# Performance work log

Measured on AMD Instinct MI355X. Metric: run time of the kernel, lower is better.

Reference implementation:

```python
import jax, jax.numpy as jnp
import numpy as np

N_NODES = 100000
N_EDGES = 3200000
D_FEAT = 32


def setup_inputs() -> dict:
    key = jax.random.key(0)
    k1, k2, k3 = jax.random.split(key, 3)
    inp = jax.random.normal(k1, (N_NODES, D_FEAT), dtype=jnp.float32)
    eidx = jax.random.randint(k2, (2, N_EDGES), 0, N_NODES, dtype=jnp.int64)
    enorm = jax.random.uniform(k3, (N_EDGES,), dtype=jnp.float32)
    esgn = jnp.ones((N_EDGES,), dtype=jnp.float32)
    return {"input": inp, "eidx": eidx, "enorm": enorm, "esgn": esgn}


def reference(input, eidx, enorm, esgn):
    # Gather source node features, scale by sign * norm, scatter-add to targets.
    sidx, tidx = eidx[0], eidx[1]
    message = input[sidx] * (esgn * enorm)[:, None]  # [n_edges, d]
    res = jax.ops.segment_sum(message, tidx, num_segments=input.shape[0])
    return res.astype(input.dtype)
```

## Files before the change

### kernel.cpp

```cpp
#include <hip/hip_runtime.h>


#define G    256
#define KMAX 1024
#define SPAN_SHIFT 7
#define SPAN 128
#define CAP  6144
#define NB   256

__global__ __launch_bounds__(1024) void hist_kernel(
    const int* __restrict__ tidx, int* __restrict__ cnt,
    int n_edges, int epb, int vec)
{
    __shared__ int lh[KMAX];
    int g = blockIdx.x, t = threadIdx.x;
    lh[t] = 0;
    __syncthreads();
    int beg = g * epb;
    int lim = beg + epb; if (lim > n_edges) lim = n_edges;
    if (vec) {
        int nq = (lim > beg) ? ((lim - beg) >> 2) : 0;
        for (int q = t; q < nq; q += 1024) {
            int4 tn = *(const int4*)(tidx + beg + q * 4);
            atomicAdd(&lh[tn.x >> SPAN_SHIFT], 1);
            atomicAdd(&lh[tn.y >> SPAN_SHIFT], 1);
            atomicAdd(&lh[tn.z >> SPAN_SHIFT], 1);
            atomicAdd(&lh[tn.w >> SPAN_SHIFT], 1);
        }
        for (int e = beg + (nq << 2) + t; e < lim; e += 1024)
            atomicAdd(&lh[tidx[e] >> SPAN_SHIFT], 1);
    } else {
        for (int e = beg + t; e < lim; e += 1024)
            atomicAdd(&lh[tidx[e] >> SPAN_SHIFT], 1);
    }
    __syncthreads();
    cnt[g * KMAX + t] = lh[t];
}

__global__ __launch_bounds__(G) void scan1_kernel(
    const int* __restrict__ cnt, int* __restrict__ pref, int* __restrict__ tot)
{
    __shared__ int part[G];
    int b = blockIdx.x, t = threadIdx.x;
    int c = cnt[t * KMAX + b];
    part[t] = c;
    __syncthreads();
    for (int off = 1; off < G; off <<= 1) {
        int v = (t >= off) ? part[t - off] : 0;
        __syncthreads();
        part[t] += v;
        __syncthreads();
    }
    pref[t * KMAX + b] = part[t] - c;
    if (t == G - 1) tot[b] = part[t];
}

__global__ __launch_bounds__(KMAX) void bscan_kernel(
    const int* __restrict__ tot, int* __restrict__ bbase)
{
    __shared__ int part[KMAX];
    int t = threadIdx.x;
    int c = tot[t];
    part[t] = c;
    __syncthreads();
    for (int off = 1; off < KMAX; off <<= 1) {
        int v = (t >= off) ? part[t - off] : 0;
        __syncthreads();
        part[t] += v;
        __syncthreads();
    }
    bbase[t] = part[t] - c;
    if (t == KMAX - 1) bbase[KMAX] = part[t];
}

__global__ __launch_bounds__(1024) void scatter_kernel(
    const int* __restrict__ sidx, const int* __restrict__ tidx,
    const float* __restrict__ enorm, const float* __restrict__ esgn,
    const int* __restrict__ bbase, const int* __restrict__ pref,
    int2* __restrict__ recs, int n_edges, int epb, int vec)
{
    __shared__ int gbase[KMAX];
    __shared__ int lh[KMAX];
    int g = blockIdx.x, t = threadIdx.x;
    gbase[t] = bbase[t] + pref[g * KMAX + t];
    lh[t] = 0;
    __syncthreads();
    int beg = g * epb;
    int lim = beg + epb; if (lim > n_edges) lim = n_edges;

    #define SCAT_EDGE(tn_, sn_, w_) {                                        \
        int b_ = (tn_) >> SPAN_SHIFT;                                        \
        int rank_ = atomicAdd(&lh[b_], 1);                                   \
        unsigned rec_ = ((unsigned)(sn_) << SPAN_SHIFT) |                    \
                        (unsigned)((tn_) & (SPAN - 1));                      \
        recs[gbase[b_] + rank_] = make_int2((int)rec_, __float_as_int(w_)); }

    if (vec) {
        int nq = (lim > beg) ? ((lim - beg) >> 2) : 0;
        for (int q = t; q < nq; q += 1024) {
            int e = beg + q * 4;
            int4   tn = *(const int4*)(tidx + e);
            int4   sn = *(const int4*)(sidx + e);
            float4 nw = *(const float4*)(enorm + e);
            float4 sw = *(const float4*)(esgn + e);
            SCAT_EDGE(tn.x, sn.x, nw.x * sw.x);
            SCAT_EDGE(tn.y, sn.y, nw.y * sw.y);
            SCAT_EDGE(tn.z, sn.z, nw.z * sw.z);
            SCAT_EDGE(tn.w, sn.w, nw.w * sw.w);
        }
        for (int e = beg + (nq << 2) + t; e < lim; e += 1024) {
            int tn = tidx[e]; int sn = sidx[e];
            float w = enorm[e] * esgn[e];
            SCAT_EDGE(tn, sn, w);
        }
    } else {
        for (int e = beg + t; e < lim; e += 1024) {
            int tn = tidx[e]; int sn = sidx[e];
            float w = enorm[e] * esgn[e];
            SCAT_EDGE(tn, sn, w);
        }
    }
    #undef SCAT_EDGE
}

__global__ __launch_bounds__(1024) void bucket_accum(
    const float* __restrict__ input, const int2* __restrict__ recs,
    const int* __restrict__ bbase, float* __restrict__ out, int n_nodes)
{
    __shared__ int2 srec[CAP];
    __shared__ int lcnt[SPAN];
    __shared__ int lbeg[SPAN];
    __shared__ int lcur[SPAN];
    int b = blockIdx.x;
    int t = threadIdx.x;
    int bstart = bbase[b], bend = bbase[b + 1];
    int base_node = b << SPAN_SHIFT;

    if (bend - bstart <= CAP) {
        if (t < SPAN) lcnt[t] = 0;
        __syncthreads();
        for (int i = bstart + t; i < bend; i += 1024)
            atomicAdd(&lcnt[recs[i].x & (SPAN - 1)], 1);
        __syncthreads();
        int c = (t < SPAN) ? lcnt[t] : 0;
        if (t < SPAN) lbeg[t] = c;
        __syncthreads();
        for (int off = 1; off < SPAN; off <<= 1) {
            int v = (t < SPAN && t >= off) ? lbeg[t - off] : 0;
            __syncthreads();
            if (t < SPAN) lbeg[t] += v;
            __syncthreads();
        }
        if (t < SPAN) {
            int excl = lbeg[t] - c;
            lbeg[t] = excl;
            lcur[t] = excl;
        }
        __syncthreads();
        for (int i = bstart + t; i < bend; i += 1024) {
            int2 r = recs[i];
            int pos = atomicAdd(&lcur[r.x & (SPAN - 1)], 1);
            srec[pos] = r;
        }
        __syncthreads();
        int node = t >> 3;
        int lane = t & 7;
        int beg = lbeg[node];
        int end = beg + lcnt[node];
        float4 acc = make_float4(0.f, 0.f, 0.f, 0.f);
        int i = beg;
        for (; i + 3 < end; i += 4) {
            int2 r0 = srec[i];
            int2 r1 = srec[i + 1];
            int2 r2 = srec[i + 2];
            int2 r3 = srec[i + 3];
            float4 v0 = ((const float4*)(input + (size_t)(((unsigned)r0.x) >> SPAN_SHIFT) * 32))[lane];
            float4 v1 = ((const float4*)(input + (size_t)(((unsigned)r1.x) >> SPAN_SHIFT) * 32))[lane];
            float4 v2 = ((const float4*)(input + (size_t)(((unsigned)r2.x) >> SPAN_SHIFT) * 32))[lane];
            float4 v3 = ((const float4*)(input + (size_t)(((unsigned)r3.x) >> SPAN_SHIFT) * 32))[lane];
            float w0 = __int_as_float(r0.y);
            float w1 = __int_as_float(r1.y);
            float w2 = __int_as_float(r2.y);
            float w3 = __int_as_float(r3.y);
            acc.x = fmaf(w0, v0.x, acc.x);
            acc.y = fmaf(w0, v0.y, acc.y);
            acc.z = fmaf(w0, v0.z, acc.z);
            acc.w = fmaf(w0, v0.w, acc.w);
            acc.x = fmaf(w1, v1.x, acc.x);
            acc.y = fmaf(w1, v1.y, acc.y);
            acc.z = fmaf(w1, v1.z, acc.z);
            acc.w = fmaf(w1, v1.w, acc.w);
            acc.x = fmaf(w2, v2.x, acc.x);
            acc.y = fmaf(w2, v2.y, acc.y);
            acc.z = fmaf(w2, v2.z, acc.z);
            acc.w = fmaf(w2, v2.w, acc.w);
            acc.x = fmaf(w3, v3.x, acc.x);
            acc.y = fmaf(w3, v3.y, acc.y);
            acc.z = fmaf(w3, v3.z, acc.z);
            acc.w = fmaf(w3, v3.w, acc.w);
        }
        for (; i < end; ++i) {
            int2 r = srec[i];
            float w = __int_as_float(r.y);
            float4 v = ((const float4*)(input + (size_t)(((unsigned)r.x) >> SPAN_SHIFT) * 32))[lane];
            acc.x = fmaf(w, v.x, acc.x);
            acc.y = fmaf(w, v.y, acc.y);
            acc.z = fmaf(w, v.z, acc.z);
            acc.w = fmaf(w, v.w, acc.w);
        }
        int gnode = base_node + node;
        if (gnode < n_nodes)
            ((float4*)(out + (size_t)gnode * 32))[lane] = acc;
    } else {
        for (int i = t; i < SPAN * 32; i += 1024) {
            int gn = base_node + (i >> 5);
            if (gn < n_nodes) out[(size_t)gn * 32 + (i & 31)] = 0.f;
        }
        __syncthreads();
        for (int i = bstart + t; i < bend; i += 1024) {
            int2 r = recs[i];
            float w = __int_as_float(r.y);
            int s = (int)(((unsigned)r.x) >> SPAN_SHIFT);
            int gn = base_node + (r.x & (SPAN - 1));
            if (gn < n_nodes)
                for (int j = 0; j < 32; ++j)
                    atomicAdd(&out[(size_t)gn * 32 + j], w * input[(size_t)s * 32 + j]);
        }
    }
}

__global__ __launch_bounds__(NB) void graphconv_scatter(
    const float* __restrict__ input, const int* __restrict__ sidx,
    const int* __restrict__ tidx, const float* __restrict__ enorm,
    const float* __restrict__ esgn, float* __restrict__ out, int n_edges)
{
    int t = blockIdx.x * NB + threadIdx.x;
    int e = t >> 3;
    int sub = t & 7;
    if (e >= n_edges) return;
    int s = sidx[e];
    int d = tidx[e];
    float w = enorm[e] * esgn[e];
    const float4* src = (const float4*)(input + (size_t)s * 32);
    float4 v = src[sub];
    float* op = out + (size_t)d * 32 + sub * 4;
    atomicAdd(op + 0, v.x * w);
    atomicAdd(op + 1, v.y * w);
    atomicAdd(op + 2, v.z * w);
    atomicAdd(op + 3, v.w * w);
}

extern "C" void kernel_launch(void* const* d_in, const int* in_sizes, int n_in,
                              void* d_out, int out_size, void* d_ws, size_t ws_size,
                              hipStream_t stream) {
    const float* input = (const float*)d_in[0];
    const int*   eidx  = (const int*)d_in[1];
    const float* enorm = (const float*)d_in[2];
    const float* esgn  = (const float*)d_in[3];
    float*       out   = (float*)d_out;

    int n_edges = in_sizes[1] / 2;
    int n_nodes = in_sizes[0] / 32;
    const int* sidx = eidx;
    const int* tidx = eidx + n_edges;

    int K = (n_nodes + SPAN - 1) >> SPAN_SHIFT;

    size_t need = (size_t)n_edges * 8 +
                  ((size_t)2 * G * KMAX + 2 * KMAX + 1) * 4;

    if (ws_size >= need && K <= KMAX) {
        int2* recs  = (int2*)d_ws;
        int*  cnt   = (int*)(recs + n_edges);
        int*  pref  = cnt + (size_t)G * KMAX;
        int*  tot   = pref + (size_t)G * KMAX;
        int*  bbase = tot + KMAX;

        int epb = ((n_edges + G - 1) / G + 3) & ~3;
        int vec = ((n_edges & 3) == 0 &&
                   (((uintptr_t)tidx | (uintptr_t)sidx |
                     (uintptr_t)enorm | (uintptr_t)esgn) & 15) == 0) ? 1 : 0;

        hist_kernel   <<<G,    1024, 0, stream>>>(tidx, cnt, n_edges, epb, vec);
        scan1_kernel  <<<KMAX, G,    0, stream>>>(cnt, pref, tot);
        bscan_kernel  <<<1,    KMAX, 0, stream>>>(tot, bbase);
        scatter_kernel<<<G,    1024, 0, stream>>>(sidx, tidx, enorm, esgn,
                                                  bbase, pref, recs,
                                                  n_edges, epb, vec);
        bucket_accum  <<<K,    1024, 0, stream>>>(input, recs, bbase,
                                                  out, n_nodes);
    } else {
        hipMemsetAsync(d_out, 0, (size_t)out_size * sizeof(float), stream);
        size_t threads_total = (size_t)n_edges * 8;
        int grid = (int)((threads_total + NB - 1) / NB);
        graphconv_scatter<<<grid, NB, 0, stream>>>(input, sidx, tidx, enorm, esgn,
                                                   out, n_edges);
    }
}
```

Before: 201.4 us.

## Replace per-bucket local sort with shared-memory atomic accumulation tile

The bucket accumulation kernel no longer counts, prefix-scans and reorders records per target node in shared memory. Each group of 8 threads now takes records straight from the bucket and adds weighted source features into a padded 128x33 shared-memory float tile with LDS atomics, then writes the tile out. This drops several block barriers, the local sort and the overflow fallback path, and also makes the kernel order-independent. In exchange every edge costs four float LDS atomics, which can contend when many edges hit the same target. Float summation order also becomes nondeterministic.

```diff
diff --git a/kernel.cpp b/kernel.cpp
--- a/kernel.cpp
+++ b/kernel.cpp
@@ -5,7 +5,7 @@
 #define KMAX 1024
 #define SPAN_SHIFT 7
 #define SPAN 128
-#define CAP  6144
+#define TSTRIDE 33
 #define NB   256
 
 __global__ __launch_bounds__(1024) void hist_kernel(
@@ -127,105 +127,53 @@
     const float* __restrict__ input, const int2* __restrict__ recs,
     const int* __restrict__ bbase, float* __restrict__ out, int n_nodes)
 {
-    __shared__ int2 srec[CAP];
-    __shared__ int lcnt[SPAN];
-    __shared__ int lbeg[SPAN];
-    __shared__ int lcur[SPAN];
+    __shared__ float tile[SPAN * TSTRIDE];
     int b = blockIdx.x;
     int t = threadIdx.x;
     int bstart = bbase[b], bend = bbase[b + 1];
     int base_node = b << SPAN_SHIFT;
 
-    if (bend - bstart <= CAP) {
-        if (t < SPAN) lcnt[t] = 0;
-        __syncthreads();
-        for (int i = bstart + t; i < bend; i += 1024)
-            atomicAdd(&lcnt[recs[i].x & (SPAN - 1)], 1);
-        __syncthreads();
-        int c = (t < SPAN) ? lcnt[t] : 0;
-        if (t < SPAN) lbeg[t] = c;
-        __syncthreads();
-        for (int off = 1; off < SPAN; off <<= 1) {
-            int v = (t < SPAN && t >= off) ? lbeg[t - off] : 0;
-            __syncthreads();
-            if (t < SPAN) lbeg[t] += v;
-            __syncthreads();
-        }
-        if (t < SPAN) {
-            int excl = lbeg[t] - c;
-            lbeg[t] = excl;
-            lcur[t] = excl;
-        }
-        __syncthreads();
-        for (int i = bstart + t; i < bend; i += 1024) {
-            int2 r = recs[i];
-            int pos = atomicAdd(&lcur[r.x & (SPAN - 1)], 1);
-            srec[pos] = r;
-        }
-        __syncthreads();
-        int node = t >> 3;
-        int lane = t & 7;
-        int beg = lbeg[node];
-        int end = beg + lcnt[node];
-        float4 acc = make_float4(0.f, 0.f, 0.f, 0.f);
-        int i = beg;
-        for (; i + 3 < end; i += 4) {
-            int2 r0 = srec[i];
-            int2 r1 = srec[i + 1];
-            int2 r2 = srec[i + 2];
-            int2 r3 = srec[i + 3];
-            float4 v0 = ((const float4*)(input + (size_t)(((unsigned)r0.x) >> SPAN_SHIFT) * 32))[lane];
-            float4 v1 = ((const float4*)(input + (size_t)(((unsigned)r1.x) >> SPAN_SHIFT) * 32))[lane];
-            float4 v2 = ((const float4*)(input + (size_t)(((unsigned)r2.x) >> SPAN_SHIFT) * 32))[lane];
-            float4 v3 = ((const float4*)(input + (size_t)(((unsigned)r3.x) >> SPAN_SHIFT) * 32))[lane];
-            float w0 = __int_as_float(r0.y);
-            float w1 = __int_as_float(r1.y);
-            float w2 = __int_as_float(r2.y);
-            float w3 = __int_as_float(r3.y);
-            acc.x = fmaf(w0, v0.x, acc.x);
-            acc.y = fmaf(w0, v0.y, acc.y);
-            acc.z = fmaf(w0, v0.z, acc.z);
-            acc.w = fmaf(w0, v0.w, acc.w);
-            acc.x = fmaf(w1, v1.x, acc.x);
-            acc.y = fmaf(w1, v1.y, acc.y);
-            acc.z = fmaf(w1, v1.z, acc.z);
-            acc.w = fmaf(w1, v1.w, acc.w);
-            acc.x = fmaf(w2, v2.x, acc.x);
-            acc.y = fmaf(w2, v2.y, acc.y);
-            acc.z = fmaf(w2, v2.z, acc.z);
-            acc.w = fmaf(w2, v2.w, acc.w);
-            acc.x = fmaf(w3, v3.x, acc.x);
-            acc.y = fmaf(w3, v3.y, acc.y);
-            acc.z = fmaf(w3, v3.z, acc.z);
-            acc.w = fmaf(w3, v3.w, acc.w);
-        }
-        for (; i < end; ++i) {
-            int2 r = srec[i];
-            float w = __int_as_float(r.y);
-            float4 v = ((const float4*)(input + (size_t)(((unsigned)r.x) >> SPAN_SHIFT) * 32))[lane];
-            acc.x = fmaf(w, v.x, acc.x);
-            acc.y = fmaf(w, v.y, acc.y);
-            acc.z = fmaf(w, v.z, acc.z);
-            acc.w = fmaf(w, v.w, acc.w);
-        }
-        int gnode = base_node + node;
-        if (gnode < n_nodes)
-            ((float4*)(out + (size_t)gnode * 32))[lane] = acc;
-    } else {
-        for (int i = t; i < SPAN * 32; i += 1024) {
-            int gn = base_node + (i >> 5);
-            if (gn < n_nodes) out[(size_t)gn * 32 + (i & 31)] = 0.f;
-        }
-        __syncthreads();
-        for (int i = bstart + t; i < bend; i += 1024) {
-            int2 r = recs[i];
-            float w = __int_as_float(r.y);
-            int s = (int)(((unsigned)r.x) >> SPAN_SHIFT);
-            int gn = base_node + (r.x & (SPAN - 1));
-            if (gn < n_nodes)
-                for (int j = 0; j < 32; ++j)
-                    atomicAdd(&out[(size_t)gn * 32 + j], w * input[(size_t)s * 32 + j]);
-        }
+    for (int i = t; i < SPAN * TSTRIDE; i += 1024) tile[i] = 0.f;
+    __syncthreads();
+
+    int grp  = t >> 3;
+    int lane = t & 7;
+    int slot = lane << 2;
+
+    #define ACC_EDGE(r_) {                                                   \
+        float w_ = __int_as_float((r_).y);                                   \
+        int s_ = (int)(((unsigned)(r_).x) >> SPAN_SHIFT);                    \
+        int ln_ = (r_).x & (SPAN - 1);                                       \
+        float4 v_ = ((const float4*)(input + (size_t)s_ * 32))[lane];        \
+        float* tp_ = &tile[ln_ * TSTRIDE + slot];                            \
+        atomicAdd(tp_ + 0, w_ * v_.x);                                       \
+        atomicAdd(tp_ + 1, w_ * v_.y);                                       \
+        atomicAdd(tp_ + 2, w_ * v_.z);                                       \
+        atomicAdd(tp_ + 3, w_ * v_.w); }
+
+    int i = bstart + grp;
+    for (; i + 384 < bend; i += 512) {
+        int2 r0 = recs[i];
+        int2 r1 = recs[i + 128];
+        int2 r2 = recs[i + 256];
+        int2 r3 = recs[i + 384];
+        ACC_EDGE(r0);
+        ACC_EDGE(r1);
+        ACC_EDGE(r2);
+        ACC_EDGE(r3);
+    }
+    for (; i < bend; i += 128) {
+        int2 r = recs[i];
+        ACC_EDGE(r);
+    }
+    #undef ACC_EDGE
+    __syncthreads();
+
+    for (int j = t; j < SPAN * 32; j += 1024) {
+        int node = j >> 5;
+        int gn = base_node + node;
+        if (gn < n_nodes)
+            out[(size_t)base_node * 32 + j] = tile[node * TSTRIDE + (j & 31)];
     }
 }
 
```

New measurement: 805.6 us. 4x slower.
